# Kernel tuning notes

Hardware: AMD Instinct MI355X
Metric: run time of the kernel (lower is better)

The kernel has to match this reference:

```python
import jax, jax.numpy as jnp
import numpy as np

B = 65536
SEM, COL, LAT, K, NL = 768, 64, 64, 256, 3
EPS_LN = 1e-5

def layernorm(x, g, b):
    m = jnp.mean(x, axis=-1, keepdims=True)
    v = jnp.mean((x - m) ** 2, axis=-1, keepdims=True)
    return (x - m) * jax.lax.rsqrt(v + EPS_LN) * g + b

def l2norm(x):
    n = jnp.sqrt(jnp.sum(x * x, axis=-1, keepdims=True))
    return x / jnp.maximum(n, 1e-12)

def setup_inputs() -> dict:
    key = jax.random.key(0)
    ks = jax.random.split(key, 32)
    g = lambda i, shape, s=0.02: jax.random.normal(ks[i], shape, jnp.float32) * s
    inp = {
        'semantic_emb': jax.random.normal(ks[0], (B, SEM), jnp.float32),
        'collab_emb':   jax.random.normal(ks[1], (B, COL), jnp.float32),
        # gate network: Linear(64,128)+LN+ReLU+Linear(128,64)+Sigmoid
        'gate_w1': g(2, (COL, 128)), 'gate_b1': jnp.zeros((128,)),
        'gate_ln_g': jnp.ones((128,)), 'gate_ln_b': jnp.zeros((128,)),
        'gate_w2': g(3, (128, COL)), 'gate_b2': jnp.zeros((COL,)),
        # fusion layernorm over 832
        'fusion_ln_g': jnp.ones((SEM + COL,)), 'fusion_ln_b': jnp.zeros((SEM + COL,)),
        # encoder (no bias): 832->512->256->128->64, SiLU between
        'enc_w1': g(4, (SEM + COL, 512)), 'enc_w2': g(5, (512, 256)),
        'enc_w3': g(6, (256, 128)),       'enc_w4': g(7, (128, LAT)),
        # shared decoder (no bias): 64->128->256->512, SiLU after each
        'dec_w1': g(8, (LAT, 128)), 'dec_w2': g(9, (128, 256)), 'dec_w3': g(10, (256, 512)),
        # semantic head: 512->1536 (+LN,ReLU) ->768
        'sem_w1': g(11, (512, 2 * SEM)), 'sem_b1': jnp.zeros((2 * SEM,)),
        'sem_ln_g': jnp.ones((2 * SEM,)), 'sem_ln_b': jnp.zeros((2 * SEM,)),
        'sem_w2': g(12, (2 * SEM, SEM)), 'sem_b2': jnp.zeros((SEM,)),
        # collab head: 512->256 (+LN,ReLU) ->64
        'col_w1': g(13, (512, 256)), 'col_b1': jnp.zeros((256,)),
        'col_ln_g': jnp.ones((256,)), 'col_ln_b': jnp.zeros((256,)),
        'col_w2': g(14, (256, COL)), 'col_b2': jnp.zeros((COL,)),
        # residual codebooks [n_layers, n_embed, latent_dim]
        'codebooks': jax.random.normal(ks[15], (NL, K, LAT), jnp.float32),
    }
    return inp

def _forward(semantic_emb, collab_emb, gate_w1, gate_b1, gate_ln_g, gate_ln_b,
             gate_w2, gate_b2, fusion_ln_g, fusion_ln_b,
             enc_w1, enc_w2, enc_w3, enc_w4, dec_w1, dec_w2, dec_w3,
             sem_w1, sem_b1, sem_ln_g, sem_ln_b, sem_w2, sem_b2,
             col_w1, col_b1, col_ln_g, col_ln_b, col_w2, col_b2, codebooks):
    # --- gated fusion (dropout inactive at eval) ---
    h = jax.nn.relu(layernorm(collab_emb @ gate_w1 + gate_b1, gate_ln_g, gate_ln_b))
    gate_values = jax.nn.sigmoid(h @ gate_w2 + gate_b2)
    denoised_collab = gate_values * collab_emb
    fused = layernorm(jnp.concatenate([semantic_emb, denoised_collab], axis=-1),
                      fusion_ln_g, fusion_ln_b)
    # --- encoder MLP ---
    z = jax.nn.silu(fused @ enc_w1)
    z = jax.nn.silu(z @ enc_w2)
    z = jax.nn.silu(z @ enc_w3)
    z = z @ enc_w4  # [B, LAT]
    # --- residual quantization (eval: nearest-neighbor, straight-through) ---
    residual = z
    z_q_total = jnp.zeros_like(z)
    cb_loss = jnp.float32(0.0)
    cm_loss = jnp.float32(0.0)
    codes_list = []
    for l in range(NL):
        residual = l2norm(residual)  # normalize_residuals=True
        cb = codebooks[l]  # [K, LAT]
        # argmin ||r - e||^2 == argmax (r.e - 0.5||e||^2)
        score = residual @ cb.T - 0.5 * jnp.sum(cb * cb, axis=-1)
        codes = jnp.argmax(score, axis=-1)  # [B]
        e = cb[codes]  # [B, LAT]
        cb_loss = cb_loss + jnp.mean((e - jax.lax.stop_gradient(residual)) ** 2)
        cm_loss = cm_loss + jnp.mean((jax.lax.stop_gradient(e) - residual) ** 2)
        z_q_layer = residual + jax.lax.stop_gradient(e - residual)  # straight-through
        z_q_total = z_q_total + z_q_layer
        residual = residual - z_q_layer
        codes_list.append(codes)
    codes = jnp.stack(codes_list, axis=1)  # [B, NL]
    # --- dual decoders ---
    s = jax.nn.silu(z_q_total @ dec_w1)
    s = jax.nn.silu(s @ dec_w2)
    s = jax.nn.silu(s @ dec_w3)  # [B, 512]
    sh = jax.nn.relu(layernorm(s @ sem_w1 + sem_b1, sem_ln_g, sem_ln_b))
    semantic_recon = sh @ sem_w2 + sem_b2
    ch = jax.nn.relu(layernorm(s @ col_w1 + col_b1, col_ln_g, col_ln_b))
    collab_recon = ch @ col_w2 + col_b2
    return semantic_recon, collab_recon, z_q_total, codes, cb_loss, cm_loss, gate_values

def reference(semantic_emb, collab_emb, gate_w1, gate_b1, gate_ln_g, gate_ln_b,
              gate_w2, gate_b2, fusion_ln_g, fusion_ln_b,
              enc_w1, enc_w2, enc_w3, enc_w4, dec_w1, dec_w2, dec_w3,
              sem_w1, sem_b1, sem_ln_g, sem_ln_b, sem_w2, sem_b2,
              col_w1, col_b1, col_ln_g, col_ln_b, col_w2, col_b2, codebooks):
    return _forward(semantic_emb, collab_emb, gate_w1, gate_b1, gate_ln_g, gate_ln_b,
                    gate_w2, gate_b2, fusion_ln_g, fusion_ln_b,
                    enc_w1, enc_w2, enc_w3, enc_w4, dec_w1, dec_w2, dec_w3,
                    sem_w1, sem_b1, sem_ln_g, sem_ln_b, sem_w2, sem_b2,
                    col_w1, col_b1, col_ln_g, col_ln_b, col_w2, col_b2, codebooks)
```

## Files before the change

### kernel.cpp

```cpp
#include <hip/hip_runtime.h>
#include <hip/hip_bf16.h>
#include <math.h>

typedef __bf16 bf16;
typedef __attribute__((ext_vector_type(8))) __bf16 v8bf;
typedef __attribute__((ext_vector_type(4))) float v4f;
typedef _Float16 f16;
typedef __attribute__((ext_vector_type(8))) _Float16 v8h;
typedef __attribute__((ext_vector_type(4))) _Float16 v4h;

__device__ __forceinline__ void xcd_swizzle(int& bm, int& bn) {
  const int nx = gridDim.x;
  const int id = blockIdx.y * nx + blockIdx.x;
  const int slot = id >> 3;
  const int row_in = slot / nx;
  const int bmi = (id & 7) * (gridDim.y >> 3) + row_in;
  const int bni = slot - row_in * nx;
  bm = bmi << 7; bn = bni << 7;
}

__device__ __forceinline__ void xcd_swizzle256(int& bm, int& bn) {
  const int nx = gridDim.x;
  const int id = blockIdx.y * nx + blockIdx.x;
  const int slot = id >> 3;
  const int row_in = slot / nx;
  const int bmi = (id & 7) * (gridDim.y >> 3) + row_in;
  const int bni = slot - row_in * nx;
  bm = bmi << 8; bn = bni << 8;
}

__global__ void wconv_t(const float* __restrict__ W, bf16* __restrict__ Wt, int Kd, int Nd) {
  int e = blockIdx.x * 256 + threadIdx.x;
  if (e < Kd * Nd) {
    int k = e / Nd, n = e - k * Nd;
    Wt[n * Kd + k] = (bf16)W[e];
  }
}

__global__ void wsplit_t(const float* __restrict__ W, f16* __restrict__ W0,
                         f16* __restrict__ W1, int Kd, int Nd) {
  int e = blockIdx.x * 256 + threadIdx.x;
  if (e < Kd * Nd) {
    int k = e / Nd, n = e - k * Nd;
    float v = W[e] * 2048.0f;
    f16 h0 = (f16)v;
    f16 h1 = (f16)(v - (float)h0);
    W0[n * Kd + k] = h0;
    W1[n * Kd + k] = h1;
  }
}

__global__ void cbt_k(const float* __restrict__ cb, float* __restrict__ cbT) {
  int e = blockIdx.x * 256 + threadIdx.x;
  if (e < 3 * 256 * 64) {
    int l = e >> 14, rem = e & 16383;
    int c = rem >> 6, d = rem & 63;
    cbT[l * 16384 + d * 256 + c] = cb[e];
  }
}

__global__ void nhn_k(const float* __restrict__ cb, float* __restrict__ nhn) {
  int l = blockIdx.x, c = threadIdx.x;
  const float* p = cb + l * 16384 + c * 64;
  double s = 0.0;
  for (int d = 0; d < 64; ++d) { double v = (double)p[d]; s += v * v; }
  nhn[l * 256 + c] = (float)(-0.5 * s);
}

template <int EPI>
__global__ __launch_bounds__(256, 2) void sgemm128(
    const float* __restrict__ A, const float* __restrict__ W,
    const float* __restrict__ bias, const float* __restrict__ lng,
    const float* __restrict__ lnb, float* __restrict__ C, int N, int Kd) {
  __shared__ float As[32][132];
  __shared__ float Bs[32][128];
  const int tid = threadIdx.x;
  const int w = tid >> 6, l = tid & 63;
  int tx, ty;
  if (EPI == 2) { tx = tid & 15; ty = tid >> 4; }
  else { tx = ((w & 1) << 3) | (l & 7); ty = ((w >> 1) << 3) | (l >> 3); }
  int bm, bn;
  xcd_swizzle(bm, bn);

  float acc[8][8];
#pragma unroll
  for (int i = 0; i < 8; ++i)
#pragma unroll
    for (int j = 0; j < 8; ++j) acc[i][j] = 0.0f;

  for (int k0 = 0; k0 < Kd; k0 += 32) {
    __syncthreads();
#pragma unroll
    for (int jj = 0; jj < 4; ++jj) {
      int p = tid + 256 * jj;
      int arow = p >> 3, aks = (p & 7) << 2;
      float4 v = *(const float4*)(A + (size_t)(bm + arow) * Kd + k0 + aks);
      As[aks][arow] = v.x; As[aks + 1][arow] = v.y;
      As[aks + 2][arow] = v.z; As[aks + 3][arow] = v.w;
      int bk = p >> 5, bns = (p & 31) << 2;
      float4 u = *(const float4*)(W + (size_t)(k0 + bk) * N + bn + bns);
      *(float4*)(&Bs[bk][bns]) = u;
    }
    __syncthreads();
    float cacc[8][8];
#pragma unroll
    for (int i = 0; i < 8; ++i)
#pragma unroll
      for (int j = 0; j < 8; ++j) cacc[i][j] = 0.0f;
#pragma unroll 4
    for (int kk = 0; kk < 32; ++kk) {
      float a[8], b[8];
#pragma unroll
      for (int i = 0; i < 8; ++i) a[i] = As[kk][ty * 8 + i];
#pragma unroll
      for (int j = 0; j < 8; ++j) b[j] = Bs[kk][tx * 8 + j];
#pragma unroll
      for (int i = 0; i < 8; ++i)
#pragma unroll
        for (int j = 0; j < 8; ++j) cacc[i][j] = fmaf(a[i], b[j], cacc[i][j]);
    }
#pragma unroll
    for (int i = 0; i < 8; ++i)
#pragma unroll
      for (int j = 0; j < 8; ++j) acc[i][j] += cacc[i][j];
  }

  const int colb = bn + tx * 8;
  if (EPI == 0) {
#pragma unroll
    for (int i = 0; i < 8; ++i) {
      int row = bm + ty * 8 + i;
      float o[8];
#pragma unroll
      for (int j = 0; j < 8; ++j) { float v = acc[i][j]; o[j] = v / (1.0f + expf(-v)); }
      *(float4*)(C + (size_t)row * N + colb) = make_float4(o[0], o[1], o[2], o[3]);
      *(float4*)(C + (size_t)row * N + colb + 4) = make_float4(o[4], o[5], o[6], o[7]);
    }
  } else if (EPI == 1) {
    float bb[8];
#pragma unroll
    for (int j = 0; j < 8; ++j) bb[j] = bias[colb + j];
#pragma unroll
    for (int i = 0; i < 8; ++i) {
      int row = bm + ty * 8 + i;
      float o[8];
#pragma unroll
      for (int j = 0; j < 8; ++j) o[j] = acc[i][j] + bb[j];
      *(float4*)(C + (size_t)row * N + colb) = make_float4(o[0], o[1], o[2], o[3]);
      *(float4*)(C + (size_t)row * N + colb + 4) = make_float4(o[4], o[5], o[6], o[7]);
    }
  } else {
    float bb[8], lg[8], lb[8];
#pragma unroll
    for (int j = 0; j < 8; ++j) { bb[j] = bias[colb + j]; lg[j] = lng[colb + j]; lb[j] = lnb[colb + j]; }
#pragma unroll
    for (int i = 0; i < 8; ++i) {
      int row = bm + ty * 8 + i;
      float v[8]; float s = 0.0f;
#pragma unroll
      for (int j = 0; j < 8; ++j) { v[j] = acc[i][j] + bb[j]; s += v[j]; }
      s += __shfl_xor(s, 1); s += __shfl_xor(s, 2); s += __shfl_xor(s, 4); s += __shfl_xor(s, 8);
      float mean = s * (1.0f / 128.0f);
      float ss = 0.0f;
#pragma unroll
      for (int j = 0; j < 8; ++j) { float t = v[j] - mean; ss += t * t; }
      ss += __shfl_xor(ss, 1); ss += __shfl_xor(ss, 2); ss += __shfl_xor(ss, 4); ss += __shfl_xor(ss, 8);
      float rs = 1.0f / sqrtf(ss * (1.0f / 128.0f) + 1e-5f);
      float o[8];
#pragma unroll
      for (int j = 0; j < 8; ++j) o[j] = fmaxf((v[j] - mean) * rs * lg[j] + lb[j], 0.0f);
      *(float4*)(C + (size_t)row * N + colb) = make_float4(o[0], o[1], o[2], o[3]);
      *(float4*)(C + (size_t)row * N + colb + 4) = make_float4(o[4], o[5], o[6], o[7]);
    }
  }
}

template <int EPI>
__global__ __launch_bounds__(256, 2) void sgemm64(
    const float* __restrict__ A, const float* __restrict__ W,
    const float* __restrict__ bias, const float* __restrict__ aux,
    float* __restrict__ C, float* __restrict__ C2, int Kd) {
  __shared__ float As[32][132];
  __shared__ float Bs[32][64];
  const int tid = threadIdx.x;
  const int tx = tid & 15, ty = tid >> 4;
  const int bm = blockIdx.x << 7;

  float acc[8][4];
#pragma unroll
  for (int i = 0; i < 8; ++i)
#pragma unroll
    for (int j = 0; j < 4; ++j) acc[i][j] = 0.0f;

  for (int k0 = 0; k0 < Kd; k0 += 32) {
    __syncthreads();
#pragma unroll
    for (int jj = 0; jj < 4; ++jj) {
      int p = tid + 256 * jj;
      int arow = p >> 3, aks = (p & 7) << 2;
      float4 v = *(const float4*)(A + (size_t)(bm + arow) * Kd + k0 + aks);
      As[aks][arow] = v.x; As[aks + 1][arow] = v.y;
      As[aks + 2][arow] = v.z; As[aks + 3][arow] = v.w;
    }
#pragma unroll
    for (int jj = 0; jj < 2; ++jj) {
      int p = tid + 256 * jj;
      int bk = p >> 4, bns = (p & 15) << 2;
      float4 u = *(const float4*)(W + (size_t)(k0 + bk) * 64 + bns);
      *(float4*)(&Bs[bk][bns]) = u;
    }
    __syncthreads();
    float cacc[8][4];
#pragma unroll
    for (int i = 0; i < 8; ++i)
#pragma unroll
      for (int j = 0; j < 4; ++j) cacc[i][j] = 0.0f;
#pragma unroll 4
    for (int kk = 0; kk < 32; ++kk) {
      float a[8], b[4];
#pragma unroll
      for (int i = 0; i < 8; ++i) a[i] = As[kk][ty * 8 + i];
#pragma unroll
      for (int j = 0; j < 4; ++j) b[j] = Bs[kk][tx * 4 + j];
#pragma unroll
      for (int i = 0; i < 8; ++i)
#pragma unroll
        for (int j = 0; j < 4; ++j) cacc[i][j] = fmaf(a[i], b[j], cacc[i][j]);
    }
#pragma unroll
    for (int i = 0; i < 8; ++i)
#pragma unroll
      for (int j = 0; j < 4; ++j) acc[i][j] += cacc[i][j];
  }

  const int colb = tx * 4;
  if (EPI == 0) {
#pragma unroll
    for (int i = 0; i < 8; ++i) {
      int row = bm + ty * 8 + i;
      float ss = 0.0f;
#pragma unroll
      for (int j = 0; j < 4; ++j) ss += acc[i][j] * acc[i][j];
      ss += __shfl_xor(ss, 1); ss += __shfl_xor(ss, 2); ss += __shfl_xor(ss, 4); ss += __shfl_xor(ss, 8);
      float nrm = fmaxf(sqrtf(ss), 1e-12f);
      *(float4*)(C + (size_t)row * 64 + colb) =
          make_float4(acc[i][0] / nrm, acc[i][1] / nrm, acc[i][2] / nrm, acc[i][3] / nrm);
    }
  } else if (EPI == 1) {
    float bb[4];
#pragma unroll
    for (int j = 0; j < 4; ++j) bb[j] = bias[colb + j];
#pragma unroll
    for (int i = 0; i < 8; ++i) {
      int row = bm + ty * 8 + i;
      *(float4*)(C + (size_t)row * 64 + colb) =
          make_float4(acc[i][0] + bb[0], acc[i][1] + bb[1], acc[i][2] + bb[2], acc[i][3] + bb[3]);
    }
  } else {
    float bb[4];
#pragma unroll
    for (int j = 0; j < 4; ++j) bb[j] = bias[colb + j];
#pragma unroll
    for (int i = 0; i < 8; ++i) {
      int row = bm + ty * 8 + i;
      float4 av = *(const float4*)(aux + (size_t)row * 64 + colb);
      float g[4];
#pragma unroll
      for (int j = 0; j < 4; ++j) g[j] = 1.0f / (1.0f + expf(-(acc[i][j] + bb[j])));
      *(float4*)(C + (size_t)row * 64 + colb) = make_float4(g[0], g[1], g[2], g[3]);
      *(float4*)(C2 + (size_t)row * 64 + colb) =
          make_float4(g[0] * av.x, g[1] * av.y, g[2] * av.z, g[3] * av.w);
    }
  }
}

__global__ __launch_bounds__(256) void fuse_ln(
    const float* __restrict__ sem, const float* __restrict__ den,
    const float* __restrict__ fg, const float* __restrict__ fb,
    f16* __restrict__ fA0, f16* __restrict__ fA1) {
  const int w = threadIdx.x >> 6, l = threadIdx.x & 63;
  float fgv[13], fbv[13];
#pragma unroll
  for (int q = 0; q < 12; ++q) { fgv[q] = fg[q * 64 + l]; fbv[q] = fb[q * 64 + l]; }
  fgv[12] = fg[768 + l]; fbv[12] = fb[768 + l];
  for (int it = 0; it < 4; ++it) {
    int r = (blockIdx.x * 4 + w) * 4 + it;
    float sv[12];
#pragma unroll
    for (int q = 0; q < 12; ++q) sv[q] = sem[(size_t)r * 768 + q * 64 + l];
    float dv = den[(size_t)r * 64 + l];
    float s = dv;
#pragma unroll
    for (int q = 0; q < 12; ++q) s += sv[q];
#pragma unroll
    for (int m = 1; m < 64; m <<= 1) s += __shfl_xor(s, m, 64);
    float mean = s * (1.0f / 832.0f);
    float t0 = dv - mean;
    float ss = t0 * t0;
#pragma unroll
    for (int q = 0; q < 12; ++q) { float t = sv[q] - mean; ss += t * t; }
#pragma unroll
    for (int m = 1; m < 64; m <<= 1) ss += __shfl_xor(ss, m, 64);
    float sc = 1.0f / sqrtf(ss * (1.0f / 832.0f) + 1e-5f);
#pragma unroll
    for (int q = 0; q < 13; ++q) {
      float y = (q < 12) ? ((sv[q] - mean) * sc * fgv[q] + fbv[q])
                         : (t0 * sc * fgv[12] + fbv[12]);
      float t = y * 256.0f;
      f16 h0 = (f16)t;
      size_t idx = (size_t)r * 832 + q * 64 + l;
      fA0[idx] = h0;
      fA1[idx] = (f16)(t - (float)h0);
    }
  }
}

typedef __attribute__((address_space(3))) void lds_void_t;
typedef __attribute__((address_space(1))) const void gbl_void_t;
__device__ __forceinline__ void gl_lds16(const void* g, void* l) {
  __builtin_amdgcn_global_load_lds((gbl_void_t*)g, (lds_void_t*)l, 16, 0, 0);
}

__global__ __launch_bounds__(256, 1) void rq_all(
    const float* __restrict__ rn_in, const float* __restrict__ cbT,
    const float* __restrict__ nhn, const float* __restrict__ cbk,
    float* __restrict__ zq, float* __restrict__ codes,
    float* __restrict__ loss, bf16* __restrict__ zqb) {
  __shared__ __align__(16) float Al[64 * 64];
  __shared__ __align__(16) float Bl[64 * 256];
  __shared__ int rowbi[64];
  const int tid = threadIdx.x;
  const int w = tid >> 6, l = tid & 63;
  const int tx = tid & 31, ty = tid >> 5;
  const int r0 = blockIdx.x << 6;

#pragma unroll
  for (int j = 0; j < 4; ++j) {
    const int cb0 = (w << 6) + (j << 8);
    gl_lds16(rn_in + (size_t)r0 * 64 + cb0 * 4 + l * 4, (char*)Al + cb0 * 16);
  }

  float zqa[16];
#pragma unroll
  for (int i = 0; i < 16; ++i) zqa[i] = 0.0f;

  for (int L = 0; L < 3; ++L) {
    __syncthreads();
#pragma unroll
    for (int j = 0; j < 16; ++j) {
      const int cb0 = (w << 6) + (j << 8);
      gl_lds16(cbT + L * 16384 + cb0 * 4 + l * 4, (char*)Bl + cb0 * 16);
    }
    float nh[8];
#pragma unroll
    for (int j = 0; j < 4; ++j) {
      float2 n2 = *(const float2*)(nhn + L * 256 + j * 64 + tx * 2);
      nh[j * 2] = n2.x; nh[j * 2 + 1] = n2.y;
    }
    __syncthreads();

    float s0[8][8], s1[8][8];
#pragma unroll
    for (int i = 0; i < 8; ++i)
#pragma unroll
      for (int j = 0; j < 8; ++j) { s0[i][j] = 0.0f; s1[i][j] = 0.0f; }

#define RQ_CHUNK(S, KB)                                                        \
    for (int k4 = 0; k4 < 32; k4 += 4) {                                       \
      float4 av[8];                                                            \
      _Pragma("unroll")                                                        \
      for (int i = 0; i < 8; ++i)                                              \
        av[i] = *(const float4*)(Al + (ty * 8 + i) * 64 + (KB) + k4);          \
      _Pragma("unroll")                                                        \
      for (int kq = 0; kq < 4; ++kq) {                                         \
        float bv[8];                                                           \
        _Pragma("unroll")                                                      \
        for (int j = 0; j < 4; ++j) {                                          \
          float2 b2 = *(const float2*)(Bl + ((KB) + k4 + kq) * 256 + j * 64 + tx * 2); \
          bv[j * 2] = b2.x; bv[j * 2 + 1] = b2.y;                              \
        }                                                                      \
        _Pragma("unroll")                                                      \
        for (int i = 0; i < 8; ++i) {                                          \
          float a_ = (&av[i].x)[kq];                                           \
          _Pragma("unroll")                                                    \
          for (int j = 0; j < 8; ++j) S[i][j] = fmaf(a_, bv[j], S[i][j]);      \
        }                                                                      \
      }                                                                        \
    }
    RQ_CHUNK(s0, 0)
    RQ_CHUNK(s1, 32)
#undef RQ_CHUNK

#pragma unroll
    for (int i = 0; i < 8; ++i) {
      int r = ty * 8 + i;
      float sc[8];
#pragma unroll
      for (int j = 0; j < 8; ++j) sc[j] = (s0[i][j] + s1[i][j]) + nh[j];
      float bs = sc[0]; int bi = 2 * tx;
#pragma unroll
      for (int j = 1; j < 8; ++j) {
        int cj = (j >> 1) * 64 + 2 * tx + (j & 1);
        if (sc[j] > bs) { bs = sc[j]; bi = cj; }
      }
#pragma unroll
      for (int m = 1; m < 32; m <<= 1) {
        float os = __shfl_xor(bs, m, 64);
        int oi = __shfl_xor(bi, m, 64);
        if (os > bs || (os == bs && oi < bi)) { bs = os; bi = oi; }
      }
      if (tx == 0) {
        rowbi[r] = bi;
        codes[(size_t)(r0 + r) * 3 + L] = (float)bi;
      }
    }
    __syncthreads();

    float lacc = 0.0f;
    const float* cbkL = cbk + L * 16384;
#pragma unroll
    for (int it = 0; it < 16; ++it) {
      int r = w * 16 + it;
      float rl = Al[r * 64 + l];
      int bi = rowbi[r];
      float e = cbkL[bi * 64 + l];
      float emr = e - rl;
      float zql = rl + emr;
      lacc += emr * emr;
      if (L == 0) zqa[it] = zql; else zqa[it] += zql;
      if (L < 2) {
        float rnew = rl - zql;
        float ss = rnew * rnew;
#pragma unroll
        for (int m = 1; m < 64; m <<= 1) ss += __shfl_xor(ss, m, 64);
        float nrm = fmaxf(sqrtf(ss), 1e-12f);
        Al[r * 64 + l] = rnew / nrm;
      } else {
        float tot = zqa[it];
        zq[(size_t)(r0 + r) * 64 + l] = tot;
        zqb[(size_t)(r0 + r) * 64 + l] = (bf16)tot;
      }
    }
#pragma unroll
    for (int m = 1; m < 64; m <<= 1) lacc += __shfl_xor(lacc, m, 64);
    if (l == 0) {
      float v = lacc * (1.0f / 4194304.0f);
      atomicAdd(loss, v);
      atomicAdd(loss + 1, v);
    }
  }
}

template <int EPI>
__global__ __launch_bounds__(256, 3) void bgemm(
    const bf16* __restrict__ A, const bf16* __restrict__ Wt,
    const float* __restrict__ bias, void* __restrict__ Cv, int N, int Kd) {
  __shared__ __align__(16) bf16 As[128 * 32];
  __shared__ __align__(16) bf16 Bs[128 * 32];
  const int tid = threadIdx.x;
  const int w = tid >> 6, l = tid & 63;
  int bm, bn;
  xcd_swizzle(bm, bn);
  const int wm = (w >> 1) << 6, wn = (w & 1) << 6;

  v4f acc[4][4];
  v4f z4 = {0.0f, 0.0f, 0.0f, 0.0f};
#pragma unroll
  for (int i = 0; i < 4; ++i)
#pragma unroll
    for (int j = 0; j < 4; ++j) acc[i][j] = z4;

  const int srow = (w << 5) + (l >> 2);
  const int skc = (l & 3) << 3;
  const bf16* ga0 = A + (size_t)(bm + srow) * Kd + skc;
  const bf16* gb0 = Wt + (size_t)(bn + srow) * Kd + skc;
  char* la0 = (char*)As + (w << 11);
  char* lb0 = (char*)Bs + (w << 11);

  for (int k0 = 0; k0 < Kd; k0 += 32) {
    __syncthreads();
    gl_lds16(ga0 + k0, la0);
    gl_lds16(ga0 + (size_t)16 * Kd + k0, la0 + 1024);
    gl_lds16(gb0 + k0, lb0);
    gl_lds16(gb0 + (size_t)16 * Kd + k0, lb0 + 1024);
    __syncthreads();
    v8bf af[4], bfr[4];
#pragma unroll
    for (int f = 0; f < 4; ++f) {
      af[f] = *(const v8bf*)(As + (wm + f * 16 + (l & 15)) * 32 + ((l >> 4) << 3));
      bfr[f] = *(const v8bf*)(Bs + (wn + f * 16 + (l & 15)) * 32 + ((l >> 4) << 3));
    }
#pragma unroll
    for (int mf = 0; mf < 4; ++mf)
#pragma unroll
      for (int nf = 0; nf < 4; ++nf)
        acc[mf][nf] = __builtin_amdgcn_mfma_f32_16x16x32_bf16(af[mf], bfr[nf], acc[mf][nf], 0, 0, 0);
  }

  const int cbase = bn + wn + (l & 15);
  float bb[4];
  if (EPI != 0) {
#pragma unroll
    for (int nf = 0; nf < 4; ++nf) bb[nf] = bias[cbase + nf * 16];
  }
#pragma unroll
  for (int mf = 0; mf < 4; ++mf) {
#pragma unroll
    for (int i = 0; i < 4; ++i) {
      int row = bm + wm + mf * 16 + ((l >> 4) << 2) + i;
#pragma unroll
      for (int nf = 0; nf < 4; ++nf) {
        int col = cbase + nf * 16;
        float v = acc[mf][nf][i];
        if (EPI == 0) {
          v = v / (1.0f + __expf(-v));
          ((bf16*)Cv)[(size_t)row * N + col] = (bf16)v;
        } else if (EPI == 1) {
          v += bb[nf];
          ((bf16*)Cv)[(size_t)row * N + col] = (bf16)v;
        } else {
          v += bb[nf];
          ((float*)Cv)[(size_t)row * N + col] = v;
        }
      }
    }
  }
}

__device__ __forceinline__ void stage_plane(const f16* __restrict__ src, int Kd,
                                            int rbase, int k0, char* base,
                                            int wid, int l) {
#pragma unroll
  for (int j = 0; j < 2; ++j) {
    int Cc = wid * 128 + j * 64 + l;
    int cc = Cc ^ ((Cc >> 3) & 3);
    gl_lds16(src + (size_t)(rbase + (cc >> 2)) * Kd + k0 + (cc & 3) * 8,
             base + wid * 2048 + j * 1024);
  }
}

__device__ __forceinline__ v8h ldsfragh(const char* base, int row, int kb) {
  int p = row * 64 + kb;
  p ^= ((p >> 7) & 3) << 4;
  return *(const v8h*)(base + p);
}

template <int EPI>
__global__ __launch_bounds__(256, 3) void hgemmp(
    const f16* __restrict__ A0, const f16* __restrict__ A1,
    const f16* __restrict__ W0, const f16* __restrict__ W1,
    f16* __restrict__ O0, f16* __restrict__ O1, float* __restrict__ Cf,
    int N, int Kd) {
  __shared__ __align__(16) char smem[32768];
  const int tid = threadIdx.x;
  const int w = tid >> 6, l = tid & 63;
  int bm, bn;
  xcd_swizzle(bm, bn);
  const int wm = (w >> 1) << 6, wn = (w & 1) << 6;
  const int kb = (l >> 4) << 4;

  char* pa0 = smem;
  char* pa1 = smem + 8192;
  char* pb0 = smem + 16384;
  char* pb1 = smem + 24576;

  v4f acc[4][4];
  v4f z4 = {0.0f, 0.0f, 0.0f, 0.0f};
#pragma unroll
  for (int i = 0; i < 4; ++i)
#pragma unroll
    for (int j = 0; j < 4; ++j) acc[i][j] = z4;

  for (int k0 = 0; k0 < Kd; k0 += 32) {
    __syncthreads();
    stage_plane(A0, Kd, bm, k0, pa0, w, l);
    stage_plane(A1, Kd, bm, k0, pa1, w, l);
    stage_plane(W0, Kd, bn, k0, pb0, w, l);
    stage_plane(W1, Kd, bn, k0, pb1, w, l);
    __syncthreads();
    v8h a0f[4], a1f[4], b0f[4], b1f[4];
#pragma unroll
    for (int f = 0; f < 4; ++f) {
      a0f[f] = ldsfragh(pa0, wm + f * 16 + (l & 15), kb);
      a1f[f] = ldsfragh(pa1, wm + f * 16 + (l & 15), kb);
      b0f[f] = ldsfragh(pb0, wn + f * 16 + (l & 15), kb);
      b1f[f] = ldsfragh(pb1, wn + f * 16 + (l & 15), kb);
    }
#pragma unroll
    for (int mf = 0; mf < 4; ++mf)
#pragma unroll
      for (int nf = 0; nf < 4; ++nf) {
        acc[mf][nf] = __builtin_amdgcn_mfma_f32_16x16x32_f16(a0f[mf], b1f[nf], acc[mf][nf], 0, 0, 0);
        acc[mf][nf] = __builtin_amdgcn_mfma_f32_16x16x32_f16(a1f[mf], b0f[nf], acc[mf][nf], 0, 0, 0);
        acc[mf][nf] = __builtin_amdgcn_mfma_f32_16x16x32_f16(a0f[mf], b0f[nf], acc[mf][nf], 0, 0, 0);
      }
  }

  const float sc = 1.0f / (256.0f * 2048.0f);
  const int cbase = bn + wn + (l & 15);
#pragma unroll
  for (int mf = 0; mf < 4; ++mf) {
#pragma unroll
    for (int i = 0; i < 4; ++i) {
      int row = bm + wm + mf * 16 + ((l >> 4) << 2) + i;
#pragma unroll
      for (int nf = 0; nf < 4; ++nf) {
        int col = cbase + nf * 16;
        float v = acc[mf][nf][i] * sc;
        v = v / (1.0f + expf(-v));
        if (EPI == 0) {
          float t = v * 256.0f;
          f16 h0 = (f16)t;
          O0[(size_t)row * N + col] = h0;
          O1[(size_t)row * N + col] = (f16)(t - (float)h0);
        } else {
          Cf[(size_t)row * N + col] = v;
        }
      }
    }
  }
}

__device__ __forceinline__ void stage_half(const bf16* __restrict__ src, int Kd,
                                           int rbase, int k0, char* hb8,
                                           int wid, int l) {
#pragma unroll
  for (int j = 0; j < 2; ++j) {
    int Cc = wid * 128 + j * 64 + l;
    int cc = Cc ^ (((Cc >> 3) & 3) << 1);
    gl_lds16(src + (size_t)(rbase + (cc >> 3)) * Kd + k0 + (cc & 7) * 8,
             hb8 + wid * 2048 + j * 1024);
  }
}

__device__ __forceinline__ v8bf ldsfrag(const char* base, int row, int kb) {
  int p = row * 128 + kb;
  p ^= ((p >> 7) & 3) << 5;
  return *(const v8bf*)(base + p);
}

__device__ __forceinline__ void rd_a(v8bf (&af)[2][4], const char* ab, int mh, int l) {
  const int rb = mh * 64 + (l & 15);
  const int kb = (l >> 4) * 16;
#pragma unroll
  for (int ks = 0; ks < 2; ++ks)
#pragma unroll
    for (int mf = 0; mf < 4; ++mf)
      af[ks][mf] = ldsfrag(ab, rb + mf * 16, ks * 64 + kb);
}

__device__ __forceinline__ void rd_b(v8bf (&bfr)[2][2], const char* bbp, int nh, int wl, int l) {
  const int rb = wl + nh * 32 + (l & 15);
  const int kb = (l >> 4) * 16;
#pragma unroll
  for (int ks = 0; ks < 2; ++ks)
#pragma unroll
    for (int nf = 0; nf < 2; ++nf)
      bfr[ks][nf] = ldsfrag(bbp, rb + nf * 16, ks * 64 + kb);
}

__device__ __forceinline__ void qmfma(v4f (&q)[4][2], const v8bf (&af)[2][4],
                                      const v8bf (&bfr)[2][2]) {
  __builtin_amdgcn_s_setprio(1);
#pragma unroll
  for (int ks = 0; ks < 2; ++ks)
#pragma unroll
    for (int mf = 0; mf < 4; ++mf)
#pragma unroll
      for (int nf = 0; nf < 2; ++nf)
        q[mf][nf] = __builtin_amdgcn_mfma_f32_16x16x32_bf16(af[ks][mf], bfr[ks][nf],
                                                            q[mf][nf], 0, 0, 0);
  __builtin_amdgcn_s_setprio(0);
}

#define PHASE_BAR() do { __builtin_amdgcn_s_barrier(); __builtin_amdgcn_sched_barrier(0); } while (0)

template <int EPI>
__global__ __launch_bounds__(512, 2) void bgemm8(
    const bf16* __restrict__ A, const bf16* __restrict__ Wt,
    const float* __restrict__ bias, void* __restrict__ Cv, int N, int Kd) {
  __shared__ __align__(16) char smem[131072];
  const int tid = threadIdx.x;
  const int wid = tid >> 6, l = tid & 63;
  int bm, bn;
  xcd_swizzle256(bm, bn);
  const int ha = wid >> 2;
  const int hbv = (wid & 3) >> 1;
  const int wl = (wid & 1) * 64;
  const int NT = Kd >> 6;

  v4f acc[2][2][4][2];
  v4f z4 = {0.0f, 0.0f, 0.0f, 0.0f};
#pragma unroll
  for (int a = 0; a < 2; ++a)
#pragma unroll
    for (int b = 0; b < 2; ++b)
#pragma unroll
      for (int c = 0; c < 4; ++c)
#pragma unroll
        for (int d = 0; d < 2; ++d) acc[a][b][c][d] = z4;

  stage_half(A,  Kd, bm,       0,  smem + 0,     wid, l);
  stage_half(A,  Kd, bm + 128, 0,  smem + 16384, wid, l);
  stage_half(Wt, Kd, bn,       0,  smem + 32768, wid, l);
  stage_half(Wt, Kd, bn + 128, 0,  smem + 49152, wid, l);
  stage_half(A,  Kd, bm,       64, smem + 65536, wid, l);
  stage_half(A,  Kd, bm + 128, 64, smem + 81920, wid, l);
  asm volatile("s_waitcnt vmcnt(4)" ::: "memory");
  PHASE_BAR();

  for (int K = 0; K < NT; ++K) {
    const int cur = K & 1;
    const char* ab = smem + cur * 65536 + ha * 16384;
    const char* bb = smem + cur * 65536 + 32768 + hbv * 16384;
    char* stB = smem + ((K + 1) & 1) * 65536 + 32768;
    char* stA = smem + cur * 65536;
    const int kB = (K + 1 < NT) ? (K + 1) << 6 : 0;
    const int kA = (K + 2 < NT) ? (K + 2) << 6 : 0;
    v8bf a0[2][4], a1[2][4], b0[2][2], b1[2][2];

    rd_a(a0, ab, 0, l);
    rd_b(b0, bb, 0, wl, l);
    stage_half(Wt, Kd, bn, kB, stB, wid, l);
    PHASE_BAR();
    qmfma(acc[0][0], a0, b0);
    PHASE_BAR();
    rd_b(b1, bb, 1, wl, l);
    stage_half(Wt, Kd, bn + 128, kB, stB + 16384, wid, l);
    PHASE_BAR();
    qmfma(acc[0][1], a0, b1);
    PHASE_BAR();
    rd_a(a1, ab, 1, l);
    PHASE_BAR();
    qmfma(acc[1][0], a1, b0);
    PHASE_BAR();
    stage_half(A, Kd, bm, kA, stA, wid, l);
    stage_half(A, Kd, bm + 128, kA, stA + 16384, wid, l);
    PHASE_BAR();
    qmfma(acc[1][1], a1, b1);
    asm volatile("s_waitcnt vmcnt(4)" ::: "memory");
    PHASE_BAR();
  }
  asm volatile("s_waitcnt vmcnt(0)" ::: "memory");

  const int r0 = bm + ha * 128 + ((l >> 4) << 2);
  const int c0 = bn + (wid & 3) * 64 + (l & 15);
  float bb4[2][2];
  if (EPI != 0) {
#pragma unroll
    for (int nh = 0; nh < 2; ++nh)
#pragma unroll
      for (int nf = 0; nf < 2; ++nf) bb4[nh][nf] = bias[c0 + nh * 32 + nf * 16];
  }
#pragma unroll
  for (int mh = 0; mh < 2; ++mh)
#pragma unroll
    for (int mf = 0; mf < 4; ++mf)
#pragma unroll
      for (int i = 0; i < 4; ++i) {
        const int row = r0 + mh * 64 + mf * 16 + i;
#pragma unroll
        for (int nh = 0; nh < 2; ++nh)
#pragma unroll
          for (int nf = 0; nf < 2; ++nf) {
            const int col = c0 + nh * 32 + nf * 16;
            float v = acc[mh][nh][mf][nf][i];
            if (EPI == 0) {
              v = v / (1.0f + __expf(-v));
              ((bf16*)Cv)[(size_t)row * N + col] = (bf16)v;
            } else if (EPI == 1) {
              v += bb4[nh][nf];
              ((bf16*)Cv)[(size_t)row * N + col] = (bf16)v;
            } else {
              v += bb4[nh][nf];
              ((float*)Cv)[(size_t)row * N + col] = v;
            }
          }
      }
}

template <int VPT, typename T>
__global__ __launch_bounds__(256) void ln_relu(T* __restrict__ x,
    const float* __restrict__ g, const float* __restrict__ b) {
  const int N = VPT * 256;
  const size_t base = (size_t)blockIdx.x * N;
  const int tid = threadIdx.x, w = tid >> 6, l = tid & 63;
  float v[VPT];
#pragma unroll
  for (int q = 0; q < VPT; ++q) v[q] = (float)x[base + q * 256 + tid];
  float s = 0.0f;
#pragma unroll
  for (int q = 0; q < VPT; ++q) s += v[q];
#pragma unroll
  for (int m = 1; m < 64; m <<= 1) s += __shfl_xor(s, m, 64);
  __shared__ float red[8];
  if (l == 0) red[w] = s;
  __syncthreads();
  float mean = (red[0] + red[1] + red[2] + red[3]) * (1.0f / N);
  float ss = 0.0f;
#pragma unroll
  for (int q = 0; q < VPT; ++q) { float t = v[q] - mean; ss += t * t; }
#pragma unroll
  for (int m = 1; m < 64; m <<= 1) ss += __shfl_xor(ss, m, 64);
  if (l == 0) red[4 + w] = ss;
  __syncthreads();
  float var = (red[4] + red[5] + red[6] + red[7]) * (1.0f / N);
  float rs = 1.0f / sqrtf(var + 1e-5f);
#pragma unroll
  for (int q = 0; q < VPT; ++q) {
    int j = q * 256 + tid;
    float y = (v[q] - mean) * rs * g[j] + b[j];
    x[base + j] = (T)fmaxf(y, 0.0f);
  }
}

extern "C" void kernel_launch(void* const* d_in, const int* in_sizes, int n_in,
                              void* d_out, int out_size, void* d_ws, size_t ws_size,
                              hipStream_t stream) {
  (void)in_sizes; (void)n_in; (void)out_size; (void)ws_size;
  const float* semI  = (const float*)d_in[0];
  const float* colI  = (const float*)d_in[1];
  const float* gw1   = (const float*)d_in[2];
  const float* gb1   = (const float*)d_in[3];
  const float* glng  = (const float*)d_in[4];
  const float* glnb  = (const float*)d_in[5];
  const float* gw2   = (const float*)d_in[6];
  const float* gb2   = (const float*)d_in[7];
  const float* fg    = (const float*)d_in[8];
  const float* fb    = (const float*)d_in[9];
  const float* ew1   = (const float*)d_in[10];
  const float* ew2   = (const float*)d_in[11];
  const float* ew3   = (const float*)d_in[12];
  const float* ew4   = (const float*)d_in[13];
  const float* dw1   = (const float*)d_in[14];
  const float* dw2   = (const float*)d_in[15];
  const float* dw3   = (const float*)d_in[16];
  const float* sw1   = (const float*)d_in[17];
  const float* sb1   = (const float*)d_in[18];
  const float* slng  = (const float*)d_in[19];
  const float* slnb  = (const float*)d_in[20];
  const float* sw2   = (const float*)d_in[21];
  const float* sb2   = (const float*)d_in[22];
  const float* cw1   = (const float*)d_in[23];
  const float* cb1   = (const float*)d_in[24];
  const float* clng  = (const float*)d_in[25];
  const float* clnb  = (const float*)d_in[26];
  const float* cw2   = (const float*)d_in[27];
  const float* cb2   = (const float*)d_in[28];
  const float* cbk   = (const float*)d_in[29];

  float* out = (float*)d_out;
  char* ws = (char*)d_ws;

  const size_t OUT_SEM = 0, OUT_COL = 50331648, OUT_ZQ = 54525952,
               OUT_CODES = 58720256, OUT_CB = 58916864, OUT_GATE = 58916866;

  bf16* dec1t = (bf16*)(ws + 0);
  bf16* dec2t = (bf16*)(ws + 16384);
  bf16* dec3t = (bf16*)(ws + 81920);
  bf16* sem1t = (bf16*)(ws + 344064);
  bf16* sem2t = (bf16*)(ws + 1916928);
  bf16* col1t = (bf16*)(ws + 4276224);
  float* cbT  = (float*)(ws + 4538368);
  float* nhn  = (float*)(ws + 4734976);
  f16* e1w0   = (f16*)(ws + 4739072);
  f16* e1w1   = (f16*)(ws + 5591040);
  f16* e2w0   = (f16*)(ws + 6443008);
  f16* e2w1   = (f16*)(ws + 6705152);
  f16* e3w0   = (f16*)(ws + 6967296);
  f16* e3w1   = (f16*)(ws + 7032832);
  const size_t WS_A = 8388608, WS_B = 226492416;
  f16* fA0 = (f16*)(ws + WS_A);
  f16* fA1 = (f16*)(ws + WS_A + 109051904);
  bf16*  semh   = (bf16*)(ws + WS_A);
  float* den = (float*)(ws + WS_B);
  float* hn  = (float*)(ws + WS_B + 16777216);
  f16* h1a = (f16*)(ws + WS_B);
  f16* h1b = (f16*)(ws + WS_B + 67108864);
  f16* h2a = (f16*)(ws + 360710144);
  f16* h2b = (f16*)(ws + 360710144 + 33554432);
  float* h3  = (float*)(ws + 427819008);
  float* rn  = (float*)(ws + 461373440);
  bf16* zqb  = (bf16*)(ws + WS_B);
  bf16* d1b  = (bf16*)(ws + WS_B + 8388608);
  bf16* d2b  = (bf16*)(ws + WS_B + 25165824);
  bf16* sb   = (bf16*)(ws + WS_B + 58720256);
  float* colh = (float*)(ws + WS_B + 125829120);

  hipMemsetAsync(out + OUT_CB, 0, 2 * sizeof(float), stream);

  wconv_t<<<(64 * 128 + 255) / 256, 256, 0, stream>>>(dw1, dec1t, 64, 128);
  wconv_t<<<(128 * 256 + 255) / 256, 256, 0, stream>>>(dw2, dec2t, 128, 256);
  wconv_t<<<(256 * 512 + 255) / 256, 256, 0, stream>>>(dw3, dec3t, 256, 512);
  wconv_t<<<(512 * 1536 + 255) / 256, 256, 0, stream>>>(sw1, sem1t, 512, 1536);
  wconv_t<<<(1536 * 768 + 255) / 256, 256, 0, stream>>>(sw2, sem2t, 1536, 768);
  wconv_t<<<(512 * 256 + 255) / 256, 256, 0, stream>>>(cw1, col1t, 512, 256);
  wsplit_t<<<(832 * 512 + 255) / 256, 256, 0, stream>>>(ew1, e1w0, e1w1, 832, 512);
  wsplit_t<<<(512 * 256 + 255) / 256, 256, 0, stream>>>(ew2, e2w0, e2w1, 512, 256);
  wsplit_t<<<(256 * 128 + 255) / 256, 256, 0, stream>>>(ew3, e3w0, e3w1, 256, 128);
  cbt_k<<<192, 256, 0, stream>>>(cbk, cbT);
  nhn_k<<<3, 256, 0, stream>>>(cbk, nhn);

  sgemm128<2><<<dim3(1, 512), 256, 0, stream>>>(colI, gw1, gb1, glng, glnb, hn, 128, 64);
  sgemm64<2><<<512, 256, 0, stream>>>(hn, gw2, gb2, colI, out + OUT_GATE, den, 128);
  fuse_ln<<<4096, 256, 0, stream>>>(semI, den, fg, fb, fA0, fA1);

  hgemmp<0><<<dim3(4, 512), 256, 0, stream>>>(fA0, fA1, e1w0, e1w1, h1a, h1b, nullptr, 512, 832);
  hgemmp<0><<<dim3(2, 512), 256, 0, stream>>>(h1a, h1b, e2w0, e2w1, h2a, h2b, nullptr, 256, 512);
  hgemmp<1><<<dim3(1, 512), 256, 0, stream>>>(h2a, h2b, e3w0, e3w1, nullptr, nullptr, h3, 128, 256);
  sgemm64<0><<<512, 256, 0, stream>>>(h3, ew4, nullptr, nullptr, rn, nullptr, 128);

  rq_all<<<1024, 256, 0, stream>>>(rn, cbT, nhn, cbk,
                                   out + OUT_ZQ, out + OUT_CODES, out + OUT_CB, zqb);

  bgemm<0><<<dim3(1, 512), 256, 0, stream>>>(zqb, dec1t, nullptr, d1b, 128, 64);
  bgemm8<0><<<dim3(1, 256), 512, 0, stream>>>(d1b, dec2t, nullptr, d2b, 256, 128);
  bgemm8<0><<<dim3(2, 256), 512, 0, stream>>>(d2b, dec3t, nullptr, sb, 512, 256);
  bgemm8<1><<<dim3(6, 256), 512, 0, stream>>>(sb, sem1t, sb1, semh, 1536, 512);
  ln_relu<6, bf16><<<65536, 256, 0, stream>>>(semh, slng, slnb);
  bgemm8<2><<<dim3(3, 256), 512, 0, stream>>>(semh, sem2t, sb2, out + OUT_SEM, 768, 1536);
  bgemm8<2><<<dim3(1, 256), 512, 0, stream>>>(sb, col1t, cb1, colh, 256, 512);
  ln_relu<1, float><<<65536, 256, 0, stream>>>(colh, clng, clnb);
  sgemm64<1><<<512, 256, 0, stream>>>(colh, cw2, cb2, nullptr, out + OUT_COL, nullptr, 256);
}
```

Baseline: 1.790 ms.

## Read RQ codebook directly from global memory and drop block barriers

The residual-quantization kernel no longer stages each layer's 64x256 transposed codebook in LDS. Threads read it straight from global memory (L2-resident) and split the 256 codes into two passes of 128 to reduce accumulator registers. Each wave now loads only its own rows of the residual tile and passes best indices between lanes with shuffles instead of shared memory. This removes all __syncthreads and cuts LDS use, allowing occupancy 3 in exchange for many more global loads in the inner loop.

```diff
diff --git a/kernel.cpp b/kernel.cpp
--- a/kernel.cpp
+++ b/kernel.cpp
@@ -321,14 +321,12 @@
   __builtin_amdgcn_global_load_lds((gbl_void_t*)g, (lds_void_t*)l, 16, 0, 0);
 }
 
-__global__ __launch_bounds__(256, 1) void rq_all(
+__global__ __launch_bounds__(256, 3) void rq_all(
     const float* __restrict__ rn_in, const float* __restrict__ cbT,
     const float* __restrict__ nhn, const float* __restrict__ cbk,
     float* __restrict__ zq, float* __restrict__ codes,
     float* __restrict__ loss, bf16* __restrict__ zqb) {
   __shared__ __align__(16) float Al[64 * 64];
-  __shared__ __align__(16) float Bl[64 * 256];
-  __shared__ int rowbi[64];
   const int tid = threadIdx.x;
   const int w = tid >> 6, l = tid & 63;
   const int tx = tid & 31, ty = tid >> 5;
@@ -336,93 +334,93 @@
 
 #pragma unroll
   for (int j = 0; j < 4; ++j) {
-    const int cb0 = (w << 6) + (j << 8);
+    const int cb0 = (w << 8) + (j << 6);
     gl_lds16(rn_in + (size_t)r0 * 64 + cb0 * 4 + l * 4, (char*)Al + cb0 * 16);
   }
+  asm volatile("s_waitcnt vmcnt(0)" ::: "memory");
 
   float zqa[16];
 #pragma unroll
   for (int i = 0; i < 16; ++i) zqa[i] = 0.0f;
 
   for (int L = 0; L < 3; ++L) {
-    __syncthreads();
-#pragma unroll
-    for (int j = 0; j < 16; ++j) {
-      const int cb0 = (w << 6) + (j << 8);
-      gl_lds16(cbT + L * 16384 + cb0 * 4 + l * 4, (char*)Bl + cb0 * 16);
-    }
-    float nh[8];
-#pragma unroll
-    for (int j = 0; j < 4; ++j) {
-      float2 n2 = *(const float2*)(nhn + L * 256 + j * 64 + tx * 2);
-      nh[j * 2] = n2.x; nh[j * 2 + 1] = n2.y;
-    }
-    __syncthreads();
-
-    float s0[8][8], s1[8][8];
-#pragma unroll
-    for (int i = 0; i < 8; ++i)
-#pragma unroll
-      for (int j = 0; j < 8; ++j) { s0[i][j] = 0.0f; s1[i][j] = 0.0f; }
+    const float* cbL = cbT + L * 16384;
+    float bs8[8]; int bi8[8];
+
+#pragma unroll
+    for (int p = 0; p < 2; ++p) {
+      float nh[4];
+#pragma unroll
+      for (int j = 0; j < 2; ++j) {
+        float2 n2 = *(const float2*)(nhn + L * 256 + p * 128 + j * 64 + tx * 2);
+        nh[j * 2] = n2.x; nh[j * 2 + 1] = n2.y;
+      }
+      float s0[8][4], s1[8][4];
+#pragma unroll
+      for (int i = 0; i < 8; ++i)
+#pragma unroll
+        for (int j = 0; j < 4; ++j) { s0[i][j] = 0.0f; s1[i][j] = 0.0f; }
 
 #define RQ_CHUNK(S, KB)                                                        \
-    for (int k4 = 0; k4 < 32; k4 += 4) {                                       \
-      float4 av[8];                                                            \
-      _Pragma("unroll")                                                        \
-      for (int i = 0; i < 8; ++i)                                              \
-        av[i] = *(const float4*)(Al + (ty * 8 + i) * 64 + (KB) + k4);          \
-      _Pragma("unroll")                                                        \
-      for (int kq = 0; kq < 4; ++kq) {                                         \
-        float bv[8];                                                           \
+      for (int k4 = 0; k4 < 32; k4 += 4) {                                     \
+        float4 av[8];                                                          \
         _Pragma("unroll")                                                      \
-        for (int j = 0; j < 4; ++j) {                                          \
-          float2 b2 = *(const float2*)(Bl + ((KB) + k4 + kq) * 256 + j * 64 + tx * 2); \
-          bv[j * 2] = b2.x; bv[j * 2 + 1] = b2.y;                              \
+        for (int i = 0; i < 8; ++i)                                            \
+          av[i] = *(const float4*)(Al + (ty * 8 + i) * 64 + (KB) + k4);        \
+        _Pragma("unroll")                                                      \
+        for (int kq = 0; kq < 4; ++kq) {                                       \
+          float bv[4];                                                         \
+          _Pragma("unroll")                                                    \
+          for (int j = 0; j < 2; ++j) {                                        \
+            float2 b2 = *(const float2*)(cbL + ((KB) + k4 + kq) * 256 +        \
+                                          p * 128 + j * 64 + tx * 2);          \
+            bv[j * 2] = b2.x; bv[j * 2 + 1] = b2.y;                            \
+          }                                                                    \
+          _Pragma("unroll")                                                    \
+          for (int i = 0; i < 8; ++i) {                                        \
+            float a_ = (&av[i].x)[kq];                                         \
+            _Pragma("unroll")                                                  \
+            for (int j = 0; j < 4; ++j) S[i][j] = fmaf(a_, bv[j], S[i][j]);    \
+          }                                                                    \
         }                                                                      \
-        _Pragma("unroll")                                                      \
-        for (int i = 0; i < 8; ++i) {                                          \
-          float a_ = (&av[i].x)[kq];                                           \
-          _Pragma("unroll")                                                    \
-          for (int j = 0; j < 8; ++j) S[i][j] = fmaf(a_, bv[j], S[i][j]);      \
-        }                                                                      \
-      }                                                                        \
-    }
-    RQ_CHUNK(s0, 0)
-    RQ_CHUNK(s1, 32)
+      }
+      RQ_CHUNK(s0, 0)
+      RQ_CHUNK(s1, 32)
 #undef RQ_CHUNK
 
 #pragma unroll
+      for (int i = 0; i < 8; ++i) {
+        float sc[4];
+#pragma unroll
+        for (int j = 0; j < 4; ++j) sc[j] = (s0[i][j] + s1[i][j]) + nh[j];
+        if (p == 0) { bs8[i] = sc[0]; bi8[i] = 2 * tx; }
+        else if (sc[0] > bs8[i]) { bs8[i] = sc[0]; bi8[i] = 128 + 2 * tx; }
+#pragma unroll
+        for (int j = 1; j < 4; ++j) {
+          int cj = p * 128 + (j >> 1) * 64 + 2 * tx + (j & 1);
+          if (sc[j] > bs8[i]) { bs8[i] = sc[j]; bi8[i] = cj; }
+        }
+      }
+    }
+
+#pragma unroll
     for (int i = 0; i < 8; ++i) {
-      int r = ty * 8 + i;
-      float sc[8];
-#pragma unroll
-      for (int j = 0; j < 8; ++j) sc[j] = (s0[i][j] + s1[i][j]) + nh[j];
-      float bs = sc[0]; int bi = 2 * tx;
-#pragma unroll
-      for (int j = 1; j < 8; ++j) {
-        int cj = (j >> 1) * 64 + 2 * tx + (j & 1);
-        if (sc[j] > bs) { bs = sc[j]; bi = cj; }
+#pragma unroll
+      for (int m = 1; m < 32; m <<= 1) {
+        float os = __shfl_xor(bs8[i], m, 64);
+        int oi = __shfl_xor(bi8[i], m, 64);
+        if (os > bs8[i] || (os == bs8[i] && oi < bi8[i])) { bs8[i] = os; bi8[i] = oi; }
       }
-#pragma unroll
-      for (int m = 1; m < 32; m <<= 1) {
-        float os = __shfl_xor(bs, m, 64);
-        int oi = __shfl_xor(bi, m, 64);
-        if (os > bs || (os == bs && oi < bi)) { bs = os; bi = oi; }
-      }
-      if (tx == 0) {
-        rowbi[r] = bi;
-        codes[(size_t)(r0 + r) * 3 + L] = (float)bi;
-      }
-    }
-    __syncthreads();
+      if (tx == 0) codes[(size_t)(r0 + ty * 8 + i) * 3 + L] = (float)bi8[i];
+    }
 
     float lacc = 0.0f;
     const float* cbkL = cbk + L * 16384;
 #pragma unroll
     for (int it = 0; it < 16; ++it) {
       int r = w * 16 + it;
+      int bi = __shfl(bi8[it & 7], (it >> 3) << 5, 64);
       float rl = Al[r * 64 + l];
-      int bi = rowbi[r];
       float e = cbkL[bi * 64 + l];
       float emr = e - rl;
       float zql = rl + emr;
```

New measurement: 2.744 ms. +53.3%, slower.
